# Kernel tuning notes

Measured on AMD Instinct MI355X. Metric: run time of the kernel, lower is better.

Reference implementation:

```python
import jax, jax.numpy as jnp
import numpy as np

TOPK = 2


def setup_inputs() -> dict:
    key = jax.random.key(0)
    k1, k2, k3, k4, k5 = jax.random.split(key, 5)
    D, H, E = 1024, 1408, 8
    hidden_states = jax.random.normal(k1, (2, 1024, D), dtype=jnp.float32)
    gate_w = jax.random.normal(k2, (E, D), dtype=jnp.float32) * 0.02
    w1g = jax.random.normal(k3, (E, D, H), dtype=jnp.float32) * 0.02
    w1u = jax.random.normal(k4, (E, D, H), dtype=jnp.float32) * 0.02
    w2 = jax.random.normal(k5, (E, H, D), dtype=jnp.float32) * 0.02
    return {"hidden_states": hidden_states, "gate_w": gate_w, "w1g": w1g, "w1u": w1u, "w2": w2}


def reference(hidden_states, gate_w, w1g, w1u, w2):
    # hidden_states: [B, S, D]; expert weights: w1g/w1u [E, D, H], w2 [E, H, D]
    B, S, D = hidden_states.shape
    E = gate_w.shape[0]
    x = hidden_states.reshape(-1, D)  # [T, D]
    T = x.shape[0]

    # --- MoEGate: softmax scores, top-k routing (no topk renorm) ---
    logits = x @ gate_w.T                      # [T, E]
    scores = jax.nn.softmax(logits, axis=-1)   # [T, E]
    topk_w, topk_idx = jax.lax.top_k(scores, TOPK)  # [T, K]

    # Per-token combine coefficient for each expert: coeff[t, e] = sum_k w[t,k] * (idx[t,k]==e)
    coeff = jnp.zeros((T, E), dtype=x.dtype).at[jnp.arange(T)[:, None], topk_idx].add(topk_w)

    # --- Grouped expert MLP (swiglu): identical math to permute + grouped GEMM + unpermute ---
    g = jnp.einsum('td,edh->teh', x, w1g)      # [T, E, H]
    u = jnp.einsum('td,edh->teh', x, w1u)      # [T, E, H]
    h = jax.nn.silu(g) * u                     # [T, E, H]
    y = jnp.einsum('teh,te,ehd->td', h, coeff, w2)  # [T, D]
    return y.reshape(B, S, D)
```

## Files before the change

kernel.cpp:

```cpp
#include <hip/hip_runtime.h>

#define TOK 2048
#define DDIM 1024
#define HDIM 1408
#define ENUM 8
#define NSLOT (2 * TOK)
#define UP_NB 22
#define UP_KS 32
#define DN_NB 16
#define DN_KS 44
#define DN_KH 22
#define TC_W1_BLK 2816
#define TC_ALL_BLK 4224
#define GATE_BLK 512

typedef unsigned int uint;
typedef unsigned short ushort;
typedef unsigned long long ull;

using bf16x8 = __attribute__((ext_vector_type(8))) __bf16;
using f32x4  = __attribute__((ext_vector_type(4))) float;

__device__ __forceinline__ float silu_f(float g) {
    return g / (1.0f + __expf(-g));
}

__device__ __forceinline__ ushort cvt_bf16(float f) {
    uint u = __float_as_uint(f);
    u += 0x7FFFu + ((u >> 16) & 1u);
    return (ushort)(u >> 16);
}

__device__ __forceinline__ void gl2lds16(const void* g, void* l) {
    __builtin_amdgcn_global_load_lds(
        (const __attribute__((address_space(1))) uint*)g,
        (__attribute__((address_space(3))) uint*)l, 16, 0, 0);
}

__global__ __launch_bounds__(256) void tcast_gate_kernel(
    const float* __restrict__ w1g, const float* __restrict__ w1u,
    const float* __restrict__ w2, ushort* __restrict__ BgP,
    ushort* __restrict__ BuP, ushort* __restrict__ W2P,
    const float* __restrict__ x, const float* __restrict__ gw,
    int* __restrict__ tinfo, float* __restrict__ wslot, ushort* __restrict__ xb)
{
    const int bid = blockIdx.x;
    const int tid = threadIdx.x;

    if (bid < TC_ALL_BLK) {
        const float* src; ushort* dst; int N, KS, NB, e, nb, ks0;
        if (bid < TC_W1_BLK) {
            const int z = bid / 176;
            const int rem = bid - z * 176;
            src = (z & 8) ? w1u : w1g;
            dst = (z & 8) ? BuP : BgP;
            N = HDIM; KS = UP_KS; NB = UP_NB; e = z & 7;
            nb = rem >> 3; ks0 = (rem & 7) * 4;
        } else {
            const int b2 = bid - TC_W1_BLK;
            e = b2 / 176;
            const int rem = b2 - e * 176;
            src = w2; dst = W2P;
            N = DDIM; KS = DN_KS; NB = DN_NB;
            nb = rem / 11; ks0 = (rem - nb * 11) * 4;
        }
        const int kg = tid & 3;
        const int nn = tid >> 2;
        const float* sb = src + (size_t)e * ((size_t)KS * 32) * N + nb * 64 + nn;
        ushort* db = dst + ((((size_t)e * NB + nb) * KS) + ks0) * 2048 + nn * 32 + kg * 8;
#pragma unroll
        for (int ksi = 0; ksi < 4; ++ksi) {
            const float* st = sb + (size_t)((ks0 + ksi) * 32 + kg * 8) * N;
            float v[8];
#pragma unroll
            for (int j = 0; j < 8; ++j) v[j] = st[(size_t)j * N];
            ushort o[8];
#pragma unroll
            for (int j = 0; j < 8; ++j) o[j] = cvt_bf16(v[j]);
            *(uint4*)(db + ksi * 2048) = *(uint4*)o;
        }
        return;
    }

    const int t = (bid - TC_ALL_BLK) * 4 + (tid >> 6);
    const int lane = tid & 63;
    const float* xr = x + (size_t)t * DDIM;
    ushort* xbr = xb + (size_t)t * DDIM;
    float xv[16];
#pragma unroll
    for (int i = 0; i < 16; ++i) xv[i] = xr[lane + 64 * i];
#pragma unroll
    for (int i = 0; i < 16; ++i) xbr[lane + 64 * i] = cvt_bf16(xv[i]);
    float logit[ENUM];
#pragma unroll
    for (int e = 0; e < ENUM; ++e) {
        const float* gr = gw + (size_t)e * DDIM;
        float acc = 0.f;
#pragma unroll
        for (int i = 0; i < 16; ++i) acc += xv[i] * gr[lane + 64 * i];
#pragma unroll
        for (int s = 32; s > 0; s >>= 1) acc += __shfl_xor(acc, s, 64);
        logit[e] = acc;
    }
    if (lane == 0) {
        float mx = logit[0];
#pragma unroll
        for (int e = 1; e < ENUM; ++e) mx = fmaxf(mx, logit[e]);
        float p[ENUM]; float se = 0.f;
#pragma unroll
        for (int e = 0; e < ENUM; ++e) { p[e] = __expf(logit[e] - mx); se += p[e]; }
        float inv = 1.0f / se;
#pragma unroll
        for (int e = 0; e < ENUM; ++e) p[e] *= inv;
        int i0 = 0;
#pragma unroll
        for (int e = 1; e < ENUM; ++e) if (p[e] > p[i0]) i0 = e;
        int i1 = (i0 == 0) ? 1 : 0;
#pragma unroll
        for (int e = 0; e < ENUM; ++e) if (e != i0 && p[e] > p[i1]) i1 = e;
        tinfo[t] = i0 | (i1 << 4);
        wslot[(t << 1)] = p[i0];
        wslot[(t << 1) | 1] = p[i1];
    }
}

__global__ __launch_bounds__(256) void gate2_kernel(
    const int* __restrict__ tinfo, int* __restrict__ counts, int* __restrict__ toks)
{
    const int e = blockIdx.x;
    const int tid = threadIdx.x;
    const int lane = tid & 63;
    __shared__ int cnt;
    if (tid == 0) cnt = 0;
    __syncthreads();
    int* te = toks + e * TOK;
    for (int t = tid; t < TOK; t += 256) {
        int info = tinfo[t];
        ull m0 = __ballot((info & 15) == e);
        if (m0) {
            int base;
            if (lane == 0) base = atomicAdd(&cnt, __popcll(m0));
            base = __shfl(base, 0, 64);
            if ((m0 >> lane) & 1)
                te[base + __popcll(m0 & ((1ull << lane) - 1))] = (t << 1);
        }
        ull m1 = __ballot((info >> 4) == e);
        if (m1) {
            int base;
            if (lane == 0) base = atomicAdd(&cnt, __popcll(m1));
            base = __shfl(base, 0, 64);
            if ((m1 >> lane) & 1)
                te[base + __popcll(m1 & ((1ull << lane) - 1))] = (t << 1) | 1;
        }
    }
    __syncthreads();
    if (tid == 0) counts[e] = cnt;
}

__global__ __launch_bounds__(256, 4) void up_mfma(
    const ushort* __restrict__ xb, const ushort* __restrict__ BgP,
    const ushort* __restrict__ BuP, const int* __restrict__ counts,
    const int* __restrict__ toks, ushort* __restrict__ Hbuf)
{
    const int e = blockIdx.z;
    const int cnt = counts[e];
    const int m0 = blockIdx.y * 128;
    if (m0 >= cnt) return;
    const int nb = blockIdx.x;
    const int tid = threadIdx.x;
    const int w = tid >> 6;
    const int lane = tid & 63;
    const int q = lane >> 4;
    const int l15 = lane & 15;
    const int wr = w >> 1;
    const int wc = w & 1;

    __shared__ ushort As[2][128][32];
    __shared__ ushort Bgs[2][64][32];
    __shared__ ushort Bus[2][64][32];
    __shared__ int rowslot[128];

    if (tid < 128) rowslot[tid] = (m0 + tid < cnt) ? toks[e * TOK + m0 + tid] : -1;
    __syncthreads();

    const int srow = w * 16 + (lane >> 2);
    const int clog = (((lane & 3) + 4 - ((srow >> 1) & 3)) & 3) * 8;
    const int as0 = rowslot[srow];
    const int as1 = rowslot[srow + 64];
    const ushort* agp0 = xb + (size_t)(as0 < 0 ? 0 : (as0 >> 1)) * DDIM + clog;
    const ushort* agp1 = xb + (size_t)(as1 < 0 ? 0 : (as1 >> 1)) * DDIM + clog;
    const size_t tb = (size_t)(e * UP_NB + nb) * UP_KS * 2048;
    const ushort* bgp = BgP + tb + srow * 32 + clog;
    const ushort* bup = BuP + tb + srow * 32 + clog;

    const int coff = ((q + (l15 >> 1)) & 3) * 8;

    f32x4 accg[4][2], accu[4][2];
#pragma unroll
    for (int i = 0; i < 4; ++i)
#pragma unroll
        for (int j = 0; j < 2; ++j) { accg[i][j] = (f32x4)0.f; accu[i][j] = (f32x4)0.f; }

#define UP_PREFETCH(KSV, B)                                        \
    {                                                              \
        gl2lds16(agp0 + (KSV) * 32, &As[B][w * 16][0]);            \
        gl2lds16(agp1 + (KSV) * 32, &As[B][64 + w * 16][0]);       \
        gl2lds16(bgp + (size_t)(KSV) * 2048, &Bgs[B][w * 16][0]);  \
        gl2lds16(bup + (size_t)(KSV) * 2048, &Bus[B][w * 16][0]);  \
    }

    UP_PREFETCH(0, 0);
    __syncthreads();

    for (int ks = 0; ks < UP_KS; ++ks) {
        const int cur = ks & 1;
        const int nxt = cur ^ 1;
        if (ks + 1 < UP_KS) UP_PREFETCH(ks + 1, nxt);

        bf16x8 a[4], bg[2], bu[2];
#pragma unroll
        for (int mi = 0; mi < 4; ++mi)
            a[mi] = *(const bf16x8*)&As[cur][wr * 64 + mi * 16 + l15][coff];
#pragma unroll
        for (int ni = 0; ni < 2; ++ni) {
            bg[ni] = *(const bf16x8*)&Bgs[cur][wc * 32 + ni * 16 + l15][coff];
            bu[ni] = *(const bf16x8*)&Bus[cur][wc * 32 + ni * 16 + l15][coff];
        }
#pragma unroll
        for (int mi = 0; mi < 4; ++mi)
#pragma unroll
            for (int ni = 0; ni < 2; ++ni) {
                accg[mi][ni] = __builtin_amdgcn_mfma_f32_16x16x32_bf16(a[mi], bg[ni], accg[mi][ni], 0, 0, 0);
                accu[mi][ni] = __builtin_amdgcn_mfma_f32_16x16x32_bf16(a[mi], bu[ni], accu[mi][ni], 0, 0, 0);
            }
        __syncthreads();
    }
#undef UP_PREFETCH

#pragma unroll
    for (int mi = 0; mi < 4; ++mi) {
#pragma unroll
        for (int r = 0; r < 4; ++r) {
            int ml = wr * 64 + mi * 16 + q * 4 + r;
            int slot = rowslot[ml];
            if (slot < 0) continue;
            ushort* hrow = Hbuf + (size_t)slot * HDIM + nb * 64 + wc * 32 + l15;
#pragma unroll
            for (int ni = 0; ni < 2; ++ni)
                hrow[ni * 16] = cvt_bf16(silu_f(accg[mi][ni][r]) * accu[mi][ni][r]);
        }
    }
}

__global__ __launch_bounds__(256, 4) void down_mfma(
    const ushort* __restrict__ Hbuf, const ushort* __restrict__ W2P,
    const int* __restrict__ counts, const int* __restrict__ toks,
    float* __restrict__ Ybuf)
{
    const int z = blockIdx.z;
    const int e = z >> 1;
    const int kh = z & 1;
    const int cnt = counts[e];
    const int m0 = blockIdx.y * 128;
    if (m0 >= cnt) return;
    const int nb = blockIdx.x;
    const int tid = threadIdx.x;
    const int w = tid >> 6;
    const int lane = tid & 63;
    const int q = lane >> 4;
    const int l15 = lane & 15;
    const int wr = w >> 1;
    const int wc = w & 1;

    __shared__ ushort As[2][128][32];
    __shared__ ushort Bs[2][128][32];
    __shared__ int rowslot[128];

    if (tid < 128) rowslot[tid] = (m0 + tid < cnt) ? toks[e * TOK + m0 + tid] : -1;
    __syncthreads();

    const int srow = w * 16 + (lane >> 2);
    const int clog = (((lane & 3) + 4 - ((srow >> 1) & 3)) & 3) * 8;
    const int as0 = rowslot[srow];
    const int as1 = rowslot[srow + 64];
    const ushort* agp0 = Hbuf + (size_t)(as0 < 0 ? 0 : as0) * HDIM + kh * (DN_KH * 32) + clog;
    const ushort* agp1 = Hbuf + (size_t)(as1 < 0 ? 0 : as1) * HDIM + kh * (DN_KH * 32) + clog;
    const int nb2 = nb * 2;
    const ushort* bp0 = W2P + ((size_t)(e * DN_NB + nb2) * DN_KS + kh * DN_KH) * 2048 + srow * 32 + clog;
    const ushort* bp1 = W2P + ((size_t)(e * DN_NB + nb2 + 1) * DN_KS + kh * DN_KH) * 2048 + srow * 32 + clog;

    const int coff = ((q + (l15 >> 1)) & 3) * 8;

    f32x4 acc[4][4];
#pragma unroll
    for (int i = 0; i < 4; ++i)
#pragma unroll
        for (int j = 0; j < 4; ++j) acc[i][j] = (f32x4)0.f;

#define DN_PREFETCH(KSV, B)                                           \
    {                                                                 \
        gl2lds16(agp0 + (KSV) * 32, &As[B][w * 16][0]);               \
        gl2lds16(agp1 + (KSV) * 32, &As[B][64 + w * 16][0]);          \
        gl2lds16(bp0 + (size_t)(KSV) * 2048, &Bs[B][w * 16][0]);      \
        gl2lds16(bp1 + (size_t)(KSV) * 2048, &Bs[B][64 + w * 16][0]); \
    }

    DN_PREFETCH(0, 0);
    __syncthreads();

    for (int ks = 0; ks < DN_KH; ++ks) {
        const int cur = ks & 1;
        const int nxt = cur ^ 1;
        if (ks + 1 < DN_KH) DN_PREFETCH(ks + 1, nxt);

        bf16x8 a[4], b[4];
#pragma unroll
        for (int mi = 0; mi < 4; ++mi)
            a[mi] = *(const bf16x8*)&As[cur][wr * 64 + mi * 16 + l15][coff];
#pragma unroll
        for (int ni = 0; ni < 4; ++ni)
            b[ni] = *(const bf16x8*)&Bs[cur][wc * 64 + ni * 16 + l15][coff];
#pragma unroll
        for (int mi = 0; mi < 4; ++mi)
#pragma unroll
            for (int ni = 0; ni < 4; ++ni)
                acc[mi][ni] = __builtin_amdgcn_mfma_f32_16x16x32_bf16(a[mi], b[ni], acc[mi][ni], 0, 0, 0);
        __syncthreads();
    }
#undef DN_PREFETCH

    float* Yp = Ybuf + (size_t)kh * NSLOT * DDIM;
#pragma unroll
    for (int mi = 0; mi < 4; ++mi) {
#pragma unroll
        for (int r = 0; r < 4; ++r) {
            int ml = wr * 64 + mi * 16 + q * 4 + r;
            int slot = rowslot[ml];
            if (slot < 0) continue;
            float* yr = Yp + (size_t)slot * DDIM + nb * 128 + wc * 64 + l15;
#pragma unroll
            for (int ni = 0; ni < 4; ++ni)
                yr[ni * 16] = acc[mi][ni][r];
        }
    }
}

__global__ __launch_bounds__(256) void combine_kernel(
    const float* __restrict__ Ybuf, const float* __restrict__ wslot,
    float* __restrict__ y)
{
    const int t = blockIdx.x;
    const int j = threadIdx.x * 4;
    const float w0 = wslot[2 * t];
    const float w1 = wslot[2 * t + 1];
    const float* y00 = Ybuf + ((size_t)2 * t) * DDIM + j;
    const float* y01 = Ybuf + ((size_t)2 * t + 1) * DDIM + j;
    const float* y10 = y00 + (size_t)NSLOT * DDIM;
    const float* y11 = y01 + (size_t)NSLOT * DDIM;
    float4 a0 = *(const float4*)y00;
    float4 b0 = *(const float4*)y01;
    float4 a1 = *(const float4*)y10;
    float4 b1 = *(const float4*)y11;
    float4 o;
    o.x = w0 * (a0.x + a1.x) + w1 * (b0.x + b1.x);
    o.y = w0 * (a0.y + a1.y) + w1 * (b0.y + b1.y);
    o.z = w0 * (a0.z + a1.z) + w1 * (b0.z + b1.z);
    o.w = w0 * (a0.w + a1.w) + w1 * (b0.w + b1.w);
    *(float4*)(y + (size_t)t * DDIM + j) = o;
}

extern "C" void kernel_launch(void* const* d_in, const int* in_sizes, int n_in,
                              void* d_out, int out_size, void* d_ws, size_t ws_size,
                              hipStream_t stream) {
    const float* x   = (const float*)d_in[0];
    const float* gw  = (const float*)d_in[1];
    const float* w1g = (const float*)d_in[2];
    const float* w1u = (const float*)d_in[3];
    const float* w2  = (const float*)d_in[4];
    float* y = (float*)d_out;
    char* ws = (char*)d_ws;

    size_t off = 0;
    int*    counts = (int*)(ws + off);   off += 256;
    int*    toks   = (int*)(ws + off);   off += (size_t)ENUM * TOK * 4;
    float*  wslot  = (float*)(ws + off); off += (size_t)NSLOT * 4;
    int*    tinfo  = (int*)(ws + off);   off += (size_t)TOK * 4;
    off = (off + 255) & ~(size_t)255;
    ushort* xb     = (ushort*)(ws + off); off += (size_t)TOK * DDIM * 2;
    size_t regA = off;
    ushort* BgP  = (ushort*)(ws + regA);
    ushort* BuP  = (ushort*)(ws + regA + (size_t)ENUM * DDIM * HDIM * 2);
    float*  Ybuf = (float*)(ws + regA);
    off = regA + (size_t)2 * ENUM * DDIM * HDIM * 2;
    ushort* W2P  = (ushort*)(ws + off);  off += (size_t)ENUM * HDIM * DDIM * 2;
    ushort* Hbuf = (ushort*)(ws + off);

    tcast_gate_kernel<<<TC_ALL_BLK + GATE_BLK, 256, 0, stream>>>(
        w1g, w1u, w2, BgP, BuP, W2P, x, gw, tinfo, wslot, xb);
    gate2_kernel<<<ENUM, 256, 0, stream>>>(tinfo, counts, toks);

    up_mfma<<<dim3(UP_NB, TOK / 128, ENUM), 256, 0, stream>>>(xb, BgP, BuP, counts, toks, Hbuf);
    down_mfma<<<dim3(DDIM / 128, TOK / 128, 16), 256, 0, stream>>>(Hbuf, W2P, counts, toks, Ybuf);
    combine_kernel<<<TOK, 256, 0, stream>>>(Ybuf, wslot, y);
}
```

Measured before the change: 256.2 us.

## Stage weight cast through LDS and overlap w2 cast with up-projection GEMM

The fp32-to-bf16 weight repack now stages a row tile in LDS so global reads are coalesced float4 loads along N, instead of strided scalar column reads. The w2 cast moves out of the first kernel into extra z-slices of the up-projection launch, so it can run alongside the expert GEMM blocks instead of before them. The cost is a larger shared-memory union in up_mfma, which may reduce occupancy, plus an extra __syncthreads in the cast path.

```diff
diff --git a/kernel.cpp b/kernel.cpp
--- a/kernel.cpp
+++ b/kernel.cpp
@@ -10,8 +10,7 @@
 #define DN_NB 16
 #define DN_KS 44
 #define DN_KH 22
-#define TC_W1_BLK 2816
-#define TC_ALL_BLK 4224
+#define W1C_BLK 5632
 #define GATE_BLK 512
 
 typedef unsigned int uint;
@@ -37,52 +36,71 @@
         (__attribute__((address_space(3))) uint*)l, 16, 0, 0);
 }
 
-__global__ __launch_bounds__(256) void tcast_gate_kernel(
+template <int CW>
+__device__ __forceinline__ void cast_body(
+    const float* __restrict__ src, ushort* __restrict__ dst,
+    int N, int KS, int NB, int e, int ks, int cgrp, int tid, float* Ls)
+{
+    const int LSTR = CW + 4;
+    const float* st = src + (size_t)e * ((size_t)KS * 32) * N + (size_t)(ks * 32) * N + cgrp * CW;
+    const int r = tid >> 3;
+    const int fc = (tid & 7) * 4;
+    const float* srow = st + (size_t)r * N + fc;
+    float* lrow = Ls + r * LSTR + fc;
+#pragma unroll
+    for (int p = 0; p < CW / 32; ++p) {
+        float4 v = *(const float4*)(srow + p * 32);
+        lrow[p * 32 + 0] = v.x; lrow[p * 32 + 1] = v.y;
+        lrow[p * 32 + 2] = v.z; lrow[p * 32 + 3] = v.w;
+    }
+    __syncthreads();
+    const int nn = tid & 63;
+    const int t2g = tid >> 6;
+    if (CW == 256) {
+        const int t2 = t2g;
+        const int nb = cgrp * 4 + t2;
+        ushort* dt = dst + ((((size_t)e * NB + nb) * KS) + ks) * 2048 + nn * 32;
+        const float* lc = Ls + t2 * 64 + nn;
+        ushort o[32];
+#pragma unroll
+        for (int j = 0; j < 32; ++j) o[j] = cvt_bf16(lc[j * LSTR]);
+#pragma unroll
+        for (int q = 0; q < 4; ++q) *(uint4*)(dt + q * 8) = *(uint4*)(o + q * 8);
+    } else {
+        const int t2 = t2g >> 1;
+        const int kg = t2g & 1;
+        const int nb = cgrp * 2 + t2;
+        ushort* dt = dst + ((((size_t)e * NB + nb) * KS) + ks) * 2048 + nn * 32 + kg * 16;
+        const float* lc = Ls + (kg * 16) * LSTR + t2 * 64 + nn;
+        ushort o[16];
+#pragma unroll
+        for (int j = 0; j < 16; ++j) o[j] = cvt_bf16(lc[j * LSTR]);
+#pragma unroll
+        for (int q = 0; q < 2; ++q) *(uint4*)(dt + q * 8) = *(uint4*)(o + q * 8);
+    }
+}
+
+__global__ __launch_bounds__(256) void w1cast_gate_kernel(
     const float* __restrict__ w1g, const float* __restrict__ w1u,
-    const float* __restrict__ w2, ushort* __restrict__ BgP,
-    ushort* __restrict__ BuP, ushort* __restrict__ W2P,
+    ushort* __restrict__ BgP, ushort* __restrict__ BuP,
     const float* __restrict__ x, const float* __restrict__ gw,
     int* __restrict__ tinfo, float* __restrict__ wslot, ushort* __restrict__ xb)
 {
+    __shared__ float Ls[32][132];
     const int bid = blockIdx.x;
     const int tid = threadIdx.x;
 
-    if (bid < TC_ALL_BLK) {
-        const float* src; ushort* dst; int N, KS, NB, e, nb, ks0;
-        if (bid < TC_W1_BLK) {
-            const int z = bid / 176;
-            const int rem = bid - z * 176;
-            src = (z & 8) ? w1u : w1g;
-            dst = (z & 8) ? BuP : BgP;
-            N = HDIM; KS = UP_KS; NB = UP_NB; e = z & 7;
-            nb = rem >> 3; ks0 = (rem & 7) * 4;
-        } else {
-            const int b2 = bid - TC_W1_BLK;
-            e = b2 / 176;
-            const int rem = b2 - e * 176;
-            src = w2; dst = W2P;
-            N = DDIM; KS = DN_KS; NB = DN_NB;
-            nb = rem / 11; ks0 = (rem - nb * 11) * 4;
-        }
-        const int kg = tid & 3;
-        const int nn = tid >> 2;
-        const float* sb = src + (size_t)e * ((size_t)KS * 32) * N + nb * 64 + nn;
-        ushort* db = dst + ((((size_t)e * NB + nb) * KS) + ks0) * 2048 + nn * 32 + kg * 8;
-#pragma unroll
-        for (int ksi = 0; ksi < 4; ++ksi) {
-            const float* st = sb + (size_t)((ks0 + ksi) * 32 + kg * 8) * N;
-            float v[8];
-#pragma unroll
-            for (int j = 0; j < 8; ++j) v[j] = st[(size_t)j * N];
-            ushort o[8];
-#pragma unroll
-            for (int j = 0; j < 8; ++j) o[j] = cvt_bf16(v[j]);
-            *(uint4*)(db + ksi * 2048) = *(uint4*)o;
-        }
+    if (bid < W1C_BLK) {
+        const int z16 = bid / 352;
+        const int rem = bid - z16 * 352;
+        const int ks = rem / 11;
+        const int cgrp = rem - ks * 11;
+        cast_body<128>((z16 & 8) ? w1u : w1g, (z16 & 8) ? BuP : BgP,
+                       HDIM, UP_KS, UP_NB, z16 & 7, ks, cgrp, tid, &Ls[0][0]);
         return;
     }
 
-    const int t = (bid - TC_ALL_BLK) * 4 + (tid >> 6);
+    const int t = (bid - W1C_BLK) * 4 + (tid >> 6);
     const int lane = tid & 63;
     const float* xr = x + (size_t)t * DDIM;
     ushort* xbr = xb + (size_t)t * DDIM;
@@ -160,14 +178,37 @@
 __global__ __launch_bounds__(256, 4) void up_mfma(
     const ushort* __restrict__ xb, const ushort* __restrict__ BgP,
     const ushort* __restrict__ BuP, const int* __restrict__ counts,
-    const int* __restrict__ toks, ushort* __restrict__ Hbuf)
-{
-    const int e = blockIdx.z;
+    const int* __restrict__ toks, ushort* __restrict__ Hbuf,
+    const float* __restrict__ w2, ushort* __restrict__ W2P)
+{
+    __shared__ union {
+        struct {
+            ushort As[2][128][32];
+            ushort Bgs[2][64][32];
+            ushort Bus[2][64][32];
+            int rowslot[128];
+        } g;
+        float Ls[32][260];
+    } sm;
+
+    const int z = blockIdx.z;
+    const int tid = threadIdx.x;
+
+    if (z < 4) {
+        const int cb = z * 352 + blockIdx.y * 22 + blockIdx.x;
+        const int e = cb / 176;
+        const int rem = cb - e * 176;
+        const int ks = rem >> 2;
+        const int cgrp = rem & 3;
+        cast_body<256>(w2, W2P, DDIM, DN_KS, DN_NB, e, ks, cgrp, tid, &sm.Ls[0][0]);
+        return;
+    }
+
+    const int e = z - 4;
     const int cnt = counts[e];
     const int m0 = blockIdx.y * 128;
     if (m0 >= cnt) return;
     const int nb = blockIdx.x;
-    const int tid = threadIdx.x;
     const int w = tid >> 6;
     const int lane = tid & 63;
     const int q = lane >> 4;
@@ -175,18 +216,13 @@
     const int wr = w >> 1;
     const int wc = w & 1;
 
-    __shared__ ushort As[2][128][32];
-    __shared__ ushort Bgs[2][64][32];
-    __shared__ ushort Bus[2][64][32];
-    __shared__ int rowslot[128];
-
-    if (tid < 128) rowslot[tid] = (m0 + tid < cnt) ? toks[e * TOK + m0 + tid] : -1;
+    if (tid < 128) sm.g.rowslot[tid] = (m0 + tid < cnt) ? toks[e * TOK + m0 + tid] : -1;
     __syncthreads();
 
     const int srow = w * 16 + (lane >> 2);
     const int clog = (((lane & 3) + 4 - ((srow >> 1) & 3)) & 3) * 8;
-    const int as0 = rowslot[srow];
-    const int as1 = rowslot[srow + 64];
+    const int as0 = sm.g.rowslot[srow];
+    const int as1 = sm.g.rowslot[srow + 64];
     const ushort* agp0 = xb + (size_t)(as0 < 0 ? 0 : (as0 >> 1)) * DDIM + clog;
     const ushort* agp1 = xb + (size_t)(as1 < 0 ? 0 : (as1 >> 1)) * DDIM + clog;
     const size_t tb = (size_t)(e * UP_NB + nb) * UP_KS * 2048;
@@ -201,12 +237,12 @@
 #pragma unroll
         for (int j = 0; j < 2; ++j) { accg[i][j] = (f32x4)0.f; accu[i][j] = (f32x4)0.f; }
 
-#define UP_PREFETCH(KSV, B)                                        \
-    {                                                              \
-        gl2lds16(agp0 + (KSV) * 32, &As[B][w * 16][0]);            \
-        gl2lds16(agp1 + (KSV) * 32, &As[B][64 + w * 16][0]);       \
-        gl2lds16(bgp + (size_t)(KSV) * 2048, &Bgs[B][w * 16][0]);  \
-        gl2lds16(bup + (size_t)(KSV) * 2048, &Bus[B][w * 16][0]);  \
+#define UP_PREFETCH(KSV, B)                                             \
+    {                                                                   \
+        gl2lds16(agp0 + (KSV) * 32, &sm.g.As[B][w * 16][0]);            \
+        gl2lds16(agp1 + (KSV) * 32, &sm.g.As[B][64 + w * 16][0]);       \
+        gl2lds16(bgp + (size_t)(KSV) * 2048, &sm.g.Bgs[B][w * 16][0]);  \
+        gl2lds16(bup + (size_t)(KSV) * 2048, &sm.g.Bus[B][w * 16][0]);  \
     }
 
     UP_PREFETCH(0, 0);
@@ -220,11 +256,11 @@
         bf16x8 a[4], bg[2], bu[2];
 #pragma unroll
         for (int mi = 0; mi < 4; ++mi)
-            a[mi] = *(const bf16x8*)&As[cur][wr * 64 + mi * 16 + l15][coff];
+            a[mi] = *(const bf16x8*)&sm.g.As[cur][wr * 64 + mi * 16 + l15][coff];
 #pragma unroll
         for (int ni = 0; ni < 2; ++ni) {
-            bg[ni] = *(const bf16x8*)&Bgs[cur][wc * 32 + ni * 16 + l15][coff];
-            bu[ni] = *(const bf16x8*)&Bus[cur][wc * 32 + ni * 16 + l15][coff];
+            bg[ni] = *(const bf16x8*)&sm.g.Bgs[cur][wc * 32 + ni * 16 + l15][coff];
+            bu[ni] = *(const bf16x8*)&sm.g.Bus[cur][wc * 32 + ni * 16 + l15][coff];
         }
 #pragma unroll
         for (int mi = 0; mi < 4; ++mi)
@@ -242,7 +278,7 @@
 #pragma unroll
         for (int r = 0; r < 4; ++r) {
             int ml = wr * 64 + mi * 16 + q * 4 + r;
-            int slot = rowslot[ml];
+            int slot = sm.g.rowslot[ml];
             if (slot < 0) continue;
             ushort* hrow = Hbuf + (size_t)slot * HDIM + nb * 64 + wc * 32 + l15;
 #pragma unroll
@@ -395,11 +431,12 @@
     ushort* W2P  = (ushort*)(ws + off);  off += (size_t)ENUM * HDIM * DDIM * 2;
     ushort* Hbuf = (ushort*)(ws + off);
 
-    tcast_gate_kernel<<<TC_ALL_BLK + GATE_BLK, 256, 0, stream>>>(
-        w1g, w1u, w2, BgP, BuP, W2P, x, gw, tinfo, wslot, xb);
+    w1cast_gate_kernel<<<W1C_BLK + GATE_BLK, 256, 0, stream>>>(
+        w1g, w1u, BgP, BuP, x, gw, tinfo, wslot, xb);
     gate2_kernel<<<ENUM, 256, 0, stream>>>(tinfo, counts, toks);
 
-    up_mfma<<<dim3(UP_NB, TOK / 128, ENUM), 256, 0, stream>>>(xb, BgP, BuP, counts, toks, Hbuf);
+    up_mfma<<<dim3(UP_NB, TOK / 128, 12), 256, 0, stream>>>(
+        xb, BgP, BuP, counts, toks, Hbuf, w2, W2P);
     down_mfma<<<dim3(DDIM / 128, TOK / 128, 16), 256, 0, stream>>>(Hbuf, W2P, counts, toks, Ybuf);
     combine_kernel<<<TOK, 256, 0, stream>>>(Ybuf, wslot, y);
 }
```

Result: slower. 289.2 us (+12.9%).

## Fuse all MoE stages into one persistent cooperative kernel with grid syncs

Applied to the files above, without the earlier changes.

Replaces the five separate kernel launches (cast+gate, routing, up GEMM, down GEMM, combine) with a single persistent cooperative kernel that loops over work items and separates the phases with grid-wide barriers. Shared memory for the up and down tiles is overlaid in a union. The aim is to remove launch gaps and tail effects between stages. In exchange the grid is capped by occupancy, so the persistent loop processes several tiles per block serially, and each grid sync adds its own cost. A fallback multi-kernel path is kept in case the cooperative launch fails.

```diff
diff --git a/kernel.cpp b/kernel.cpp
--- a/kernel.cpp
+++ b/kernel.cpp
@@ -1,4 +1,7 @@
 #include <hip/hip_runtime.h>
+#include <hip/hip_cooperative_groups.h>
+
+namespace cg = cooperative_groups;
 
 #define TOK 2048
 #define DDIM 1024
@@ -11,8 +14,11 @@
 #define DN_KS 44
 #define DN_KH 22
 #define TC_W1_BLK 2816
-#define TC_ALL_BLK 4224
-#define GATE_BLK 512
+#define CAST_ITEMS 4224
+#define GATE_ITEMS 512
+#define PH1_ITEMS (CAST_ITEMS + GATE_ITEMS)
+#define UP_TILES 2816
+#define DN_TILES 2048
 
 typedef unsigned int uint;
 typedef unsigned short ushort;
@@ -20,6 +26,20 @@
 
 using bf16x8 = __attribute__((ext_vector_type(8))) __bf16;
 using f32x4  = __attribute__((ext_vector_type(4))) float;
+
+union SMem {
+    struct {
+        ushort As[2][128][32];
+        ushort Bgs[2][64][32];
+        ushort Bus[2][64][32];
+        int rowslot[128];
+    } u;
+    struct {
+        ushort As[2][128][32];
+        ushort Bs[2][128][32];
+        int rowslot[128];
+    } d;
+};
 
 __device__ __forceinline__ float silu_f(float g) {
     return g / (1.0f + __expf(-g));
@@ -37,52 +57,48 @@
         (__attribute__((address_space(3))) uint*)l, 16, 0, 0);
 }
 
-__global__ __launch_bounds__(256) void tcast_gate_kernel(
-    const float* __restrict__ w1g, const float* __restrict__ w1u,
-    const float* __restrict__ w2, ushort* __restrict__ BgP,
-    ushort* __restrict__ BuP, ushort* __restrict__ W2P,
-    const float* __restrict__ x, const float* __restrict__ gw,
-    int* __restrict__ tinfo, float* __restrict__ wslot, ushort* __restrict__ xb)
-{
-    const int bid = blockIdx.x;
-    const int tid = threadIdx.x;
-
-    if (bid < TC_ALL_BLK) {
-        const float* src; ushort* dst; int N, KS, NB, e, nb, ks0;
-        if (bid < TC_W1_BLK) {
-            const int z = bid / 176;
-            const int rem = bid - z * 176;
-            src = (z & 8) ? w1u : w1g;
-            dst = (z & 8) ? BuP : BgP;
-            N = HDIM; KS = UP_KS; NB = UP_NB; e = z & 7;
-            nb = rem >> 3; ks0 = (rem & 7) * 4;
-        } else {
-            const int b2 = bid - TC_W1_BLK;
-            e = b2 / 176;
-            const int rem = b2 - e * 176;
-            src = w2; dst = W2P;
-            N = DDIM; KS = DN_KS; NB = DN_NB;
-            nb = rem / 11; ks0 = (rem - nb * 11) * 4;
-        }
-        const int kg = tid & 3;
-        const int nn = tid >> 2;
-        const float* sb = src + (size_t)e * ((size_t)KS * 32) * N + nb * 64 + nn;
-        ushort* db = dst + ((((size_t)e * NB + nb) * KS) + ks0) * 2048 + nn * 32 + kg * 8;
-#pragma unroll
-        for (int ksi = 0; ksi < 4; ++ksi) {
-            const float* st = sb + (size_t)((ks0 + ksi) * 32 + kg * 8) * N;
-            float v[8];
-#pragma unroll
-            for (int j = 0; j < 8; ++j) v[j] = st[(size_t)j * N];
-            ushort o[8];
-#pragma unroll
-            for (int j = 0; j < 8; ++j) o[j] = cvt_bf16(v[j]);
-            *(uint4*)(db + ksi * 2048) = *(uint4*)o;
-        }
-        return;
-    }
-
-    const int t = (bid - TC_ALL_BLK) * 4 + (tid >> 6);
+__device__ __forceinline__ void cast_item(
+    int item, int tid, const float* w1g, const float* w1u, const float* w2,
+    ushort* BgP, ushort* BuP, ushort* W2P)
+{
+    const float* src; ushort* dst; int N, KS, NB, e, nb, ks0;
+    if (item < TC_W1_BLK) {
+        const int z = item / 176;
+        const int rem = item - z * 176;
+        src = (z & 8) ? w1u : w1g;
+        dst = (z & 8) ? BuP : BgP;
+        N = HDIM; KS = UP_KS; NB = UP_NB; e = z & 7;
+        nb = rem >> 3; ks0 = (rem & 7) * 4;
+    } else {
+        const int b2 = item - TC_W1_BLK;
+        e = b2 / 176;
+        const int rem = b2 - e * 176;
+        src = w2; dst = W2P;
+        N = DDIM; KS = DN_KS; NB = DN_NB;
+        nb = rem / 11; ks0 = (rem - nb * 11) * 4;
+    }
+    const int kg = tid & 3;
+    const int nn = tid >> 2;
+    const float* sb = src + (size_t)e * ((size_t)KS * 32) * N + nb * 64 + nn;
+    ushort* db = dst + ((((size_t)e * NB + nb) * KS) + ks0) * 2048 + nn * 32 + kg * 8;
+#pragma unroll
+    for (int ksi = 0; ksi < 4; ++ksi) {
+        const float* st = sb + (size_t)((ks0 + ksi) * 32 + kg * 8) * N;
+        float v[8];
+#pragma unroll
+        for (int j = 0; j < 8; ++j) v[j] = st[(size_t)j * N];
+        ushort o[8];
+#pragma unroll
+        for (int j = 0; j < 8; ++j) o[j] = cvt_bf16(v[j]);
+        *(uint4*)(db + ksi * 2048) = *(uint4*)o;
+    }
+}
+
+__device__ __forceinline__ void gate_item(
+    int item, int tid, const float* x, const float* gw,
+    int* tinfo, float* wslot, ushort* xb)
+{
+    const int t = item * 4 + (tid >> 6);
     const int lane = tid & 63;
     const float* xr = x + (size_t)t * DDIM;
     ushort* xbr = xb + (size_t)t * DDIM;
@@ -124,50 +140,66 @@
     }
 }
 
-__global__ __launch_bounds__(256) void gate2_kernel(
-    const int* __restrict__ tinfo, int* __restrict__ counts, int* __restrict__ toks)
-{
-    const int e = blockIdx.x;
-    const int tid = threadIdx.x;
+__device__ __forceinline__ void phase1(
+    int bid, int gdim, int tid,
+    const float* w1g, const float* w1u, const float* w2,
+    ushort* BgP, ushort* BuP, ushort* W2P,
+    const float* x, const float* gw,
+    int* tinfo, float* wslot, ushort* xb)
+{
+    for (int item = bid; item < PH1_ITEMS; item += gdim) {
+        if (item < CAST_ITEMS) cast_item(item, tid, w1g, w1u, w2, BgP, BuP, W2P);
+        else gate_item(item - CAST_ITEMS, tid, x, gw, tinfo, wslot, xb);
+    }
+}
+
+__device__ __forceinline__ void phase2(
+    int bid, int gdim, int tid,
+    const int* tinfo, int* counts, int* toks)
+{
+    __shared__ int s_cnt;
     const int lane = tid & 63;
-    __shared__ int cnt;
-    if (tid == 0) cnt = 0;
-    __syncthreads();
-    int* te = toks + e * TOK;
-    for (int t = tid; t < TOK; t += 256) {
-        int info = tinfo[t];
-        ull m0 = __ballot((info & 15) == e);
-        if (m0) {
-            int base;
-            if (lane == 0) base = atomicAdd(&cnt, __popcll(m0));
-            base = __shfl(base, 0, 64);
-            if ((m0 >> lane) & 1)
-                te[base + __popcll(m0 & ((1ull << lane) - 1))] = (t << 1);
+    for (int e = bid; e < ENUM; e += gdim) {
+        if (tid == 0) s_cnt = 0;
+        __syncthreads();
+        int* te = toks + e * TOK;
+        for (int t = tid; t < TOK; t += 256) {
+            int info = tinfo[t];
+            ull m0 = __ballot((info & 15) == e);
+            if (m0) {
+                int base;
+                if (lane == 0) base = atomicAdd(&s_cnt, __popcll(m0));
+                base = __shfl(base, 0, 64);
+                if ((m0 >> lane) & 1)
+                    te[base + __popcll(m0 & ((1ull << lane) - 1))] = (t << 1);
+            }
+            ull m1 = __ballot((info >> 4) == e);
+            if (m1) {
+                int base;
+                if (lane == 0) base = atomicAdd(&s_cnt, __popcll(m1));
+                base = __shfl(base, 0, 64);
+                if ((m1 >> lane) & 1)
+                    te[base + __popcll(m1 & ((1ull << lane) - 1))] = (t << 1) | 1;
+            }
         }
-        ull m1 = __ballot((info >> 4) == e);
-        if (m1) {
-            int base;
-            if (lane == 0) base = atomicAdd(&cnt, __popcll(m1));
-            base = __shfl(base, 0, 64);
-            if ((m1 >> lane) & 1)
-                te[base + __popcll(m1 & ((1ull << lane) - 1))] = (t << 1) | 1;
-        }
-    }
-    __syncthreads();
-    if (tid == 0) counts[e] = cnt;
-}
-
-__global__ __launch_bounds__(256, 4) void up_mfma(
-    const ushort* __restrict__ xb, const ushort* __restrict__ BgP,
-    const ushort* __restrict__ BuP, const int* __restrict__ counts,
-    const int* __restrict__ toks, ushort* __restrict__ Hbuf)
-{
-    const int e = blockIdx.z;
+        __syncthreads();
+        if (tid == 0) counts[e] = s_cnt;
+        __syncthreads();
+    }
+}
+
+__device__ __forceinline__ void up_tile(
+    SMem* sm, int vt, int tid,
+    const ushort* xb, const ushort* BgP, const ushort* BuP,
+    const int* counts, const int* toks, ushort* Hbuf)
+{
+    const int e = vt / 352;
+    const int rem = vt - e * 352;
+    const int my = rem / 22;
+    const int nb = rem - my * 22;
     const int cnt = counts[e];
-    const int m0 = blockIdx.y * 128;
+    const int m0 = my * 128;
     if (m0 >= cnt) return;
-    const int nb = blockIdx.x;
-    const int tid = threadIdx.x;
     const int w = tid >> 6;
     const int lane = tid & 63;
     const int q = lane >> 4;
@@ -175,18 +207,14 @@
     const int wr = w >> 1;
     const int wc = w & 1;
 
-    __shared__ ushort As[2][128][32];
-    __shared__ ushort Bgs[2][64][32];
-    __shared__ ushort Bus[2][64][32];
-    __shared__ int rowslot[128];
-
-    if (tid < 128) rowslot[tid] = (m0 + tid < cnt) ? toks[e * TOK + m0 + tid] : -1;
+    __syncthreads();
+    if (tid < 128) sm->u.rowslot[tid] = (m0 + tid < cnt) ? toks[e * TOK + m0 + tid] : -1;
     __syncthreads();
 
     const int srow = w * 16 + (lane >> 2);
     const int clog = (((lane & 3) + 4 - ((srow >> 1) & 3)) & 3) * 8;
-    const int as0 = rowslot[srow];
-    const int as1 = rowslot[srow + 64];
+    const int as0 = sm->u.rowslot[srow];
+    const int as1 = sm->u.rowslot[srow + 64];
     const ushort* agp0 = xb + (size_t)(as0 < 0 ? 0 : (as0 >> 1)) * DDIM + clog;
     const ushort* agp1 = xb + (size_t)(as1 < 0 ? 0 : (as1 >> 1)) * DDIM + clog;
     const size_t tb = (size_t)(e * UP_NB + nb) * UP_KS * 2048;
@@ -201,12 +229,12 @@
 #pragma unroll
         for (int j = 0; j < 2; ++j) { accg[i][j] = (f32x4)0.f; accu[i][j] = (f32x4)0.f; }
 
-#define UP_PREFETCH(KSV, B)                                        \
-    {                                                              \
-        gl2lds16(agp0 + (KSV) * 32, &As[B][w * 16][0]);            \
-        gl2lds16(agp1 + (KSV) * 32, &As[B][64 + w * 16][0]);       \
-        gl2lds16(bgp + (size_t)(KSV) * 2048, &Bgs[B][w * 16][0]);  \
-        gl2lds16(bup + (size_t)(KSV) * 2048, &Bus[B][w * 16][0]);  \
+#define UP_PREFETCH(KSV, B)                                              \
+    {                                                                    \
+        gl2lds16(agp0 + (KSV) * 32, &sm->u.As[B][w * 16][0]);            \
+        gl2lds16(agp1 + (KSV) * 32, &sm->u.As[B][64 + w * 16][0]);       \
+        gl2lds16(bgp + (size_t)(KSV) * 2048, &sm->u.Bgs[B][w * 16][0]);  \
+        gl2lds16(bup + (size_t)(KSV) * 2048, &sm->u.Bus[B][w * 16][0]);  \
     }
 
     UP_PREFETCH(0, 0);
@@ -220,11 +248,11 @@
         bf16x8 a[4], bg[2], bu[2];
 #pragma unroll
         for (int mi = 0; mi < 4; ++mi)
-            a[mi] = *(const bf16x8*)&As[cur][wr * 64 + mi * 16 + l15][coff];
+            a[mi] = *(const bf16x8*)&sm->u.As[cur][wr * 64 + mi * 16 + l15][coff];
 #pragma unroll
         for (int ni = 0; ni < 2; ++ni) {
-            bg[ni] = *(const bf16x8*)&Bgs[cur][wc * 32 + ni * 16 + l15][coff];
-            bu[ni] = *(const bf16x8*)&Bus[cur][wc * 32 + ni * 16 + l15][coff];
+            bg[ni] = *(const bf16x8*)&sm->u.Bgs[cur][wc * 32 + ni * 16 + l15][coff];
+            bu[ni] = *(const bf16x8*)&sm->u.Bus[cur][wc * 32 + ni * 16 + l15][coff];
         }
 #pragma unroll
         for (int mi = 0; mi < 4; ++mi)
@@ -242,7 +270,7 @@
 #pragma unroll
         for (int r = 0; r < 4; ++r) {
             int ml = wr * 64 + mi * 16 + q * 4 + r;
-            int slot = rowslot[ml];
+            int slot = sm->u.rowslot[ml];
             if (slot < 0) continue;
             ushort* hrow = Hbuf + (size_t)slot * HDIM + nb * 64 + wc * 32 + l15;
 #pragma unroll
@@ -252,19 +280,20 @@
     }
 }
 
-__global__ __launch_bounds__(256, 4) void down_mfma(
-    const ushort* __restrict__ Hbuf, const ushort* __restrict__ W2P,
-    const int* __restrict__ counts, const int* __restrict__ toks,
-    float* __restrict__ Ybuf)
-{
-    const int z = blockIdx.z;
+__device__ __forceinline__ void down_tile(
+    SMem* sm, int vt, int tid,
+    const ushort* Hbuf, const ushort* W2P,
+    const int* counts, const int* toks, float* Ybuf)
+{
+    const int z = vt / 128;
+    const int rem = vt - z * 128;
+    const int my = rem >> 3;
+    const int nb = rem & 7;
     const int e = z >> 1;
     const int kh = z & 1;
     const int cnt = counts[e];
-    const int m0 = blockIdx.y * 128;
+    const int m0 = my * 128;
     if (m0 >= cnt) return;
-    const int nb = blockIdx.x;
-    const int tid = threadIdx.x;
     const int w = tid >> 6;
     const int lane = tid & 63;
     const int q = lane >> 4;
@@ -272,17 +301,14 @@
     const int wr = w >> 1;
     const int wc = w & 1;
 
-    __shared__ ushort As[2][128][32];
-    __shared__ ushort Bs[2][128][32];
-    __shared__ int rowslot[128];
-
-    if (tid < 128) rowslot[tid] = (m0 + tid < cnt) ? toks[e * TOK + m0 + tid] : -1;
+    __syncthreads();
+    if (tid < 128) sm->d.rowslot[tid] = (m0 + tid < cnt) ? toks[e * TOK + m0 + tid] : -1;
     __syncthreads();
 
     const int srow = w * 16 + (lane >> 2);
     const int clog = (((lane & 3) + 4 - ((srow >> 1) & 3)) & 3) * 8;
-    const int as0 = rowslot[srow];
-    const int as1 = rowslot[srow + 64];
+    const int as0 = sm->d.rowslot[srow];
+    const int as1 = sm->d.rowslot[srow + 64];
     const ushort* agp0 = Hbuf + (size_t)(as0 < 0 ? 0 : as0) * HDIM + kh * (DN_KH * 32) + clog;
     const ushort* agp1 = Hbuf + (size_t)(as1 < 0 ? 0 : as1) * HDIM + kh * (DN_KH * 32) + clog;
     const int nb2 = nb * 2;
@@ -297,12 +323,12 @@
 #pragma unroll
         for (int j = 0; j < 4; ++j) acc[i][j] = (f32x4)0.f;
 
-#define DN_PREFETCH(KSV, B)                                           \
-    {                                                                 \
-        gl2lds16(agp0 + (KSV) * 32, &As[B][w * 16][0]);               \
-        gl2lds16(agp1 + (KSV) * 32, &As[B][64 + w * 16][0]);          \
-        gl2lds16(bp0 + (size_t)(KSV) * 2048, &Bs[B][w * 16][0]);      \
-        gl2lds16(bp1 + (size_t)(KSV) * 2048, &Bs[B][64 + w * 16][0]); \
+#define DN_PREFETCH(KSV, B)                                                 \
+    {                                                                       \
+        gl2lds16(agp0 + (KSV) * 32, &sm->d.As[B][w * 16][0]);               \
+        gl2lds16(agp1 + (KSV) * 32, &sm->d.As[B][64 + w * 16][0]);          \
+        gl2lds16(bp0 + (size_t)(KSV) * 2048, &sm->d.Bs[B][w * 16][0]);      \
+        gl2lds16(bp1 + (size_t)(KSV) * 2048, &sm->d.Bs[B][64 + w * 16][0]); \
     }
 
     DN_PREFETCH(0, 0);
@@ -316,10 +342,10 @@
         bf16x8 a[4], b[4];
 #pragma unroll
         for (int mi = 0; mi < 4; ++mi)
-            a[mi] = *(const bf16x8*)&As[cur][wr * 64 + mi * 16 + l15][coff];
+            a[mi] = *(const bf16x8*)&sm->d.As[cur][wr * 64 + mi * 16 + l15][coff];
 #pragma unroll
         for (int ni = 0; ni < 4; ++ni)
-            b[ni] = *(const bf16x8*)&Bs[cur][wc * 64 + ni * 16 + l15][coff];
+            b[ni] = *(const bf16x8*)&sm->d.Bs[cur][wc * 64 + ni * 16 + l15][coff];
 #pragma unroll
         for (int mi = 0; mi < 4; ++mi)
 #pragma unroll
@@ -335,7 +361,7 @@
 #pragma unroll
         for (int r = 0; r < 4; ++r) {
             int ml = wr * 64 + mi * 16 + q * 4 + r;
-            int slot = rowslot[ml];
+            int slot = sm->d.rowslot[ml];
             if (slot < 0) continue;
             float* yr = Yp + (size_t)slot * DDIM + nb * 128 + wc * 64 + l15;
 #pragma unroll
@@ -345,28 +371,93 @@
     }
 }
 
-__global__ __launch_bounds__(256) void combine_kernel(
-    const float* __restrict__ Ybuf, const float* __restrict__ wslot,
-    float* __restrict__ y)
-{
-    const int t = blockIdx.x;
-    const int j = threadIdx.x * 4;
-    const float w0 = wslot[2 * t];
-    const float w1 = wslot[2 * t + 1];
-    const float* y00 = Ybuf + ((size_t)2 * t) * DDIM + j;
-    const float* y01 = Ybuf + ((size_t)2 * t + 1) * DDIM + j;
-    const float* y10 = y00 + (size_t)NSLOT * DDIM;
-    const float* y11 = y01 + (size_t)NSLOT * DDIM;
-    float4 a0 = *(const float4*)y00;
-    float4 b0 = *(const float4*)y01;
-    float4 a1 = *(const float4*)y10;
-    float4 b1 = *(const float4*)y11;
-    float4 o;
-    o.x = w0 * (a0.x + a1.x) + w1 * (b0.x + b1.x);
-    o.y = w0 * (a0.y + a1.y) + w1 * (b0.y + b1.y);
-    o.z = w0 * (a0.z + a1.z) + w1 * (b0.z + b1.z);
-    o.w = w0 * (a0.w + a1.w) + w1 * (b0.w + b1.w);
-    *(float4*)(y + (size_t)t * DDIM + j) = o;
+__device__ __forceinline__ void phase5(
+    int bid, int gdim, int tid,
+    const float* Ybuf, const float* wslot, float* y)
+{
+    const int j = tid * 4;
+    for (int t = bid; t < TOK; t += gdim) {
+        const float w0 = wslot[2 * t];
+        const float w1 = wslot[2 * t + 1];
+        const float* y00 = Ybuf + ((size_t)2 * t) * DDIM + j;
+        const float* y01 = Ybuf + ((size_t)2 * t + 1) * DDIM + j;
+        const float* y10 = y00 + (size_t)NSLOT * DDIM;
+        const float* y11 = y01 + (size_t)NSLOT * DDIM;
+        float4 a0 = *(const float4*)y00;
+        float4 b0 = *(const float4*)y01;
+        float4 a1 = *(const float4*)y10;
+        float4 b1 = *(const float4*)y11;
+        float4 o;
+        o.x = w0 * (a0.x + a1.x) + w1 * (b0.x + b1.x);
+        o.y = w0 * (a0.y + a1.y) + w1 * (b0.y + b1.y);
+        o.z = w0 * (a0.z + a1.z) + w1 * (b0.z + b1.z);
+        o.w = w0 * (a0.w + a1.w) + w1 * (b0.w + b1.w);
+        *(float4*)(y + (size_t)t * DDIM + j) = o;
+    }
+}
+
+__global__ __launch_bounds__(256, 4) void moe_coop(
+    const float* w1g, const float* w1u, const float* w2,
+    const float* x, const float* gw,
+    ushort* BgP, ushort* BuP, ushort* W2P,
+    int* tinfo, float* wslot, ushort* xb,
+    int* counts, int* toks, ushort* Hbuf, float* Ybuf, float* y)
+{
+    __shared__ SMem sm;
+    const int tid = threadIdx.x;
+    const int bid = blockIdx.x;
+    const int gdim = gridDim.x;
+    cg::grid_group grid = cg::this_grid();
+
+    phase1(bid, gdim, tid, w1g, w1u, w2, BgP, BuP, W2P, x, gw, tinfo, wslot, xb);
+    grid.sync();
+    phase2(bid, gdim, tid, tinfo, counts, toks);
+    grid.sync();
+    for (int vt = bid; vt < UP_TILES; vt += gdim)
+        up_tile(&sm, vt, tid, xb, BgP, BuP, counts, toks, Hbuf);
+    grid.sync();
+    for (int vt = bid; vt < DN_TILES; vt += gdim)
+        down_tile(&sm, vt, tid, Hbuf, W2P, counts, toks, Ybuf);
+    grid.sync();
+    phase5(bid, gdim, tid, Ybuf, wslot, y);
+}
+
+__global__ __launch_bounds__(256) void k_ph1(
+    const float* w1g, const float* w1u, const float* w2,
+    ushort* BgP, ushort* BuP, ushort* W2P,
+    const float* x, const float* gw, int* tinfo, float* wslot, ushort* xb)
+{
+    phase1(blockIdx.x, gridDim.x, threadIdx.x, w1g, w1u, w2, BgP, BuP, W2P, x, gw, tinfo, wslot, xb);
+}
+
+__global__ __launch_bounds__(256) void k_ph2(
+    const int* tinfo, int* counts, int* toks)
+{
+    phase2(blockIdx.x, gridDim.x, threadIdx.x, tinfo, counts, toks);
+}
+
+__global__ __launch_bounds__(256, 4) void k_up(
+    const ushort* xb, const ushort* BgP, const ushort* BuP,
+    const int* counts, const int* toks, ushort* Hbuf)
+{
+    __shared__ SMem sm;
+    for (int vt = blockIdx.x; vt < UP_TILES; vt += gridDim.x)
+        up_tile(&sm, vt, threadIdx.x, xb, BgP, BuP, counts, toks, Hbuf);
+}
+
+__global__ __launch_bounds__(256, 4) void k_dn(
+    const ushort* Hbuf, const ushort* W2P,
+    const int* counts, const int* toks, float* Ybuf)
+{
+    __shared__ SMem sm;
+    for (int vt = blockIdx.x; vt < DN_TILES; vt += gridDim.x)
+        down_tile(&sm, vt, threadIdx.x, Hbuf, W2P, counts, toks, Ybuf);
+}
+
+__global__ __launch_bounds__(256) void k_cb(
+    const float* Ybuf, const float* wslot, float* y)
+{
+    phase5(blockIdx.x, gridDim.x, threadIdx.x, Ybuf, wslot, y);
 }
 
 extern "C" void kernel_launch(void* const* d_in, const int* in_sizes, int n_in,
@@ -395,11 +486,29 @@
     ushort* W2P  = (ushort*)(ws + off);  off += (size_t)ENUM * HDIM * DDIM * 2;
     ushort* Hbuf = (ushort*)(ws + off);
 
-    tcast_gate_kernel<<<TC_ALL_BLK + GATE_BLK, 256, 0, stream>>>(
-        w1g, w1u, w2, BgP, BuP, W2P, x, gw, tinfo, wslot, xb);
-    gate2_kernel<<<ENUM, 256, 0, stream>>>(tinfo, counts, toks);
-
-    up_mfma<<<dim3(UP_NB, TOK / 128, ENUM), 256, 0, stream>>>(xb, BgP, BuP, counts, toks, Hbuf);
-    down_mfma<<<dim3(DDIM / 128, TOK / 128, 16), 256, 0, stream>>>(Hbuf, W2P, counts, toks, Ybuf);
-    combine_kernel<<<TOK, 256, 0, stream>>>(Ybuf, wslot, y);
-}
+    int occ = 0;
+    hipError_t qe = hipOccupancyMaxActiveBlocksPerMultiprocessor(
+        &occ, (const void*)moe_coop, 256, 0);
+    bool done = false;
+    if (qe == hipSuccess && occ > 0) {
+        int grid = occ * 256;
+        if (grid > UP_TILES) grid = UP_TILES;
+        void* args[] = {
+            (void*)&w1g, (void*)&w1u, (void*)&w2, (void*)&x, (void*)&gw,
+            (void*)&BgP, (void*)&BuP, (void*)&W2P,
+            (void*)&tinfo, (void*)&wslot, (void*)&xb,
+            (void*)&counts, (void*)&toks, (void*)&Hbuf, (void*)&Ybuf, (void*)&y
+        };
+        if (hipLaunchCooperativeKernel((const void*)moe_coop, dim3(grid), dim3(256),
+                                       args, 0, stream) == hipSuccess)
+            done = true;
+    }
+
+    if (!done) {
+        k_ph1<<<PH1_ITEMS, 256, 0, stream>>>(w1g, w1u, w2, BgP, BuP, W2P, x, gw, tinfo, wslot, xb);
+        k_ph2<<<ENUM, 256, 0, stream>>>(tinfo, counts, toks);
+        k_up<<<UP_TILES, 256, 0, stream>>>(xb, BgP, BuP, counts, toks, Hbuf);
+        k_dn<<<DN_TILES, 256, 0, stream>>>(Hbuf, W2P, counts, toks, Ybuf);
+        k_cb<<<TOK, 256, 0, stream>>>(Ybuf, wslot, y);
+    }
+}
```

After: 739.7 us. 189% more time.
